# Kernel optimization log

Measured on AMD Instinct MI355X. Metric: run time of the kernel, lower is better.

The kernel has to match this reference:

```python
import jax, jax.numpy as jnp
import numpy as np

OUT, IN, GS = 11008, 4096, 128   # out_features, in_features, group_size
G = IN // GS                     # num_groups = 32 (in_features divisible by group_size)
TOKENS = 8192                    # batch 4 * seq 2048


def setup_inputs() -> dict:
    key = jax.random.key(0)
    k1, k2, k3, k4, k5 = jax.random.split(key, 5)
    x = jax.random.normal(k1, (TOKENS, IN), dtype=jnp.float32)
    # packed int4 weights: two nibbles per byte, stored as int32 in [0,256)
    qweight = jax.random.randint(k2, (OUT, IN // 2), 0, 256, dtype=jnp.int32)
    # realistic GPTQ scales (small positive) and zero-points in [0,15]
    scales = jax.random.uniform(k3, (OUT, G), dtype=jnp.float32) * 0.01 + 1e-3
    zeros = jax.random.uniform(k4, (OUT, G), dtype=jnp.float32) * 15.0
    bias = jax.random.normal(k5, (OUT,), dtype=jnp.float32) * 0.01
    return {"x": x, "qweight": qweight, "scales": scales, "zeros": zeros, "bias": bias}


def _dequant(qweight, scales, zeros):
    # unpack: column 2i = low nibble, column 2i+1 = high nibble (matches torch loop)
    low = (qweight & 15).astype(jnp.float32)          # [OUT, IN/2]
    high = ((qweight >> 4) & 15).astype(jnp.float32)  # [OUT, IN/2]
    w = jnp.stack([low, high], axis=-1).reshape(OUT, IN)
    # group-wise dequant: (q - zero) * scale per group of GS input channels
    w = (w.reshape(OUT, G, GS) - zeros[:, :, None]) * scales[:, :, None]
    return w.reshape(OUT, IN)


def reference(x, qweight, scales, zeros, bias):
    w = _dequant(qweight, scales, zeros)   # [OUT, IN] fp32
    # F.linear: x @ w.T + bias
    return jnp.einsum('ti,oi->to', x, w) + bias
```

## Files before the change

kernel.cpp:

```cpp
#include <hip/hip_runtime.h>
#include <stdint.h>

#define OUTF 11008
#define INF  4096
#define NG   32
#define TOK  8192
#define KB4  2048

#define BM 256
#define BN 256
#define BK 64
#define NT (INF / BK)
#define GX (OUTF / BN)
#define GY (TOK / BM)
#define NWG (GX * GY)

typedef unsigned short u16;
typedef __attribute__((ext_vector_type(8))) short bf16x8;
typedef __attribute__((ext_vector_type(4))) float f32x4;

__device__ inline u16 f2bf(float f) {
  union { float f; uint32_t u; } v; v.f = f;
  return (u16)((v.u + 0x7fff + ((v.u >> 16) & 1)) >> 16);
}

__device__ inline void async_copy16(const void* g, const void* l) {
  __builtin_amdgcn_global_load_lds(
      (__attribute__((address_space(1))) void*)(g),
      (__attribute__((address_space(3))) void*)(l), 16, 0, 0);
}

#define FENCE() asm volatile("" ::: "memory")
#define BAR()   do { FENCE(); __builtin_amdgcn_s_barrier(); FENCE(); } while (0)
#define VMCNT(n) asm volatile("s_waitcnt vmcnt(" #n ")" ::: "memory")


__global__ void dequant_w(const int* __restrict__ QW, const float* __restrict__ scales,
                          const float* __restrict__ zeros, u16* __restrict__ Wb) {
  const int idx = blockIdx.x * 256 + threadIdx.x;
  const int e = idx * 8;
  const int o = e >> 11;
  const int c = e & (KB4 - 1);
  const int g = c >> 6;
  const float s = scales[o * NG + g];
  const float z = zeros[o * NG + g];
  const float zs = -z * s;
#pragma unroll
  for (int h = 0; h < 2; ++h) {
    const int4 q = *(const int4*)(QW + (size_t)o * KB4 + c + h * 4);
    const int qq[4] = {q.x, q.y, q.z, q.w};
    union { u16 t[8]; int4 v; } u;
#pragma unroll
    for (int j = 0; j < 4; ++j) {
      u.t[2 * j]     = f2bf(fmaf((float)(qq[j] & 15), s, zs));
      u.t[2 * j + 1] = f2bf(fmaf((float)((qq[j] >> 4) & 15), s, zs));
    }
    *(int4*)(Wb + (size_t)o * INF + 2 * (c + h * 4)) = u.v;
  }
}

__global__ void cvt_x(const float* __restrict__ X, u16* __restrict__ Xb) {
  const size_t base = ((size_t)blockIdx.x * 256 + threadIdx.x) * 16;
#pragma unroll
  for (int h = 0; h < 2; ++h) {
    const float4 a = *(const float4*)(X + base + h * 8);
    const float4 b = *(const float4*)(X + base + h * 8 + 4);
    union { u16 t[8]; int4 v; } u;
    u.t[0] = f2bf(a.x); u.t[1] = f2bf(a.y); u.t[2] = f2bf(a.z); u.t[3] = f2bf(a.w);
    u.t[4] = f2bf(b.x); u.t[5] = f2bf(b.y); u.t[6] = f2bf(b.z); u.t[7] = f2bf(b.w);
    *(int4*)(Xb + base + h * 8) = u.v;
  }
}


__global__ __launch_bounds__(512, 2) void gemm_pre512(const u16* __restrict__ A,
                                                      const u16* __restrict__ B,
                                                      const float* __restrict__ bias,
                                                      float* __restrict__ C) {
  __shared__ __align__(16) u16 As[2][BM * BK];
  __shared__ __align__(16) u16 Bs[2][BN * BK];
  const int tid = threadIdx.x;
  const int lane = tid & 63;
  const int wid = __builtin_amdgcn_readfirstlane(tid >> 6);

  const int lin = blockIdx.x;
  const int wg = (lin & 7) * (NWG / 8) + (lin >> 3);
  const int bm = wg / GX;
  const int bn = wg % GX;

  const u16* Ab = A + (size_t)bm * BM * INF;
  const u16* Bb = B + (size_t)bn * BN * INF;

  const int rowoff = tid >> 3;
  const int gran = (tid & 7) ^ (rowoff & 7);
  const u16* Asrc = Ab + (size_t)rowoff * INF + gran * 8;
  const u16* Bsrc = Bb + (size_t)rowoff * INF + gran * 8;
  const int wid8 = wid * 8;

  const int rr = lane & 15;
  const int q4 = lane >> 4;
  const int wm = wid >> 2;
  const int wn = wid & 3;

  f32x4 acc[8][4] = {};
  bf16x8 af[8][2], bfv[4][2];

#define STAGE_A(S, TT)                                                         \
  _Pragma("unroll") for (int r0 = 0; r0 < BM; r0 += 64)                        \
    async_copy16(Asrc + (size_t)r0 * INF + (TT) * BK,                          \
                 (const char*)&As[S][0] + (r0 + wid8) * 128);
#define STAGE_B(S, TT)                                                         \
  _Pragma("unroll") for (int r0 = 0; r0 < BN; r0 += 64)                        \
    async_copy16(Bsrc + (size_t)r0 * INF + (TT) * BK,                          \
                 (const char*)&Bs[S][0] + (r0 + wid8) * 128);

#define LD_A(S, MH)                                                            \
  _Pragma("unroll") for (int mi = 0; mi < 4; ++mi)                             \
    _Pragma("unroll") for (int ks = 0; ks < 2; ++ks)                           \
      af[(MH) * 4 + mi][ks] = *(const bf16x8*)&As[S][                          \
          (wm * 128 + ((MH) * 4 + mi) * 16 + rr) * BK +                        \
          (((ks * 4 + q4) ^ (rr & 7)) * 8)];
#define LD_B(S, NH)                                                            \
  _Pragma("unroll") for (int ni = 0; ni < 2; ++ni)                             \
    _Pragma("unroll") for (int ks = 0; ks < 2; ++ks)                           \
      bfv[(NH) * 2 + ni][ks] = *(const bf16x8*)&Bs[S][                         \
          (wn * 64 + ((NH) * 2 + ni) * 16 + rr) * BK +                         \
          (((ks * 4 + q4) ^ (rr & 7)) * 8)];

#define MFMAQ(MH, NH)                                                          \
  do {                                                                         \
    __builtin_amdgcn_s_setprio(1);                                             \
    _Pragma("unroll") for (int ks = 0; ks < 2; ++ks)                           \
      _Pragma("unroll") for (int mi = 0; mi < 4; ++mi)                         \
        _Pragma("unroll") for (int ni = 0; ni < 2; ++ni)                       \
          acc[(MH) * 4 + mi][(NH) * 2 + ni] =                                  \
              __builtin_amdgcn_mfma_f32_16x16x32_bf16(                         \
                  af[(MH) * 4 + mi][ks], bfv[(NH) * 2 + ni][ks],               \
                  acc[(MH) * 4 + mi][(NH) * 2 + ni], 0, 0, 0);                 \
    __builtin_amdgcn_s_setprio(0);                                             \
  } while (0)

#define TILE(S, T)                                                             \
  do {                                                                         \
    LD_A(S, 0); LD_B(S, 0);                                                    \
    BAR(); MFMAQ(0, 0); BAR();                                                 \
    LD_A(S, 1); LD_B(S, 1);                                                    \
    BAR(); MFMAQ(0, 1); BAR();                                                 \
    if ((T) < NT - 2) { STAGE_A(S, (T) + 2); }                                 \
    BAR(); MFMAQ(1, 0); BAR();                                                 \
    if ((T) < NT - 2) { STAGE_B(S, (T) + 2); VMCNT(8); } else { VMCNT(0); }    \
    BAR(); MFMAQ(1, 1); BAR();                                                 \
  } while (0)

  STAGE_A(0, 0); STAGE_B(0, 0);
  STAGE_A(1, 1); STAGE_B(1, 1);
  VMCNT(8);
  BAR();

  for (int t = 0; t < NT; t += 2) {
    TILE(0, t);
    TILE(1, t + 1);
  }

  const int ncol = lane & 15;
  const int qrow = (lane >> 4) * 4;
  float bv[4];
#pragma unroll
  for (int ni = 0; ni < 4; ++ni)
    bv[ni] = bias[bn * BN + wn * 64 + ni * 16 + ncol];
#pragma unroll
  for (int mi = 0; mi < 8; ++mi)
#pragma unroll
    for (int ni = 0; ni < 4; ++ni) {
      const int gn = bn * BN + wn * 64 + ni * 16 + ncol;
#pragma unroll
      for (int r = 0; r < 4; ++r) {
        const int gm = bm * BM + wm * 128 + mi * 16 + qrow + r;
        C[(size_t)gm * OUTF + gn] = acc[mi][ni][r] + bv[ni];
      }
    }
}


#define FBM 128
#define FBN 128

#define FMFMA_COMPUTE()                                                       \
  do {                                                                        \
    const int frr = lane & 15;                                                \
    const int fq4 = lane >> 4;                                                \
    _Pragma("unroll") for (int ks = 0; ks < 2; ++ks) {                        \
      bf16x8 fa[4], fb[4];                                                    \
      const int kk = (((ks * 4 + fq4) ^ (frr & 7)) * 8);                      \
      _Pragma("unroll") for (int i = 0; i < 4; ++i) {                         \
        fa[i] = *(const bf16x8*)&Asf[(mwave + i * 16 + frr) * BK + kk];       \
        fb[i] = *(const bf16x8*)&Bsf[(nwave + i * 16 + frr) * BK + kk];       \
      }                                                                       \
      _Pragma("unroll") for (int mi = 0; mi < 4; ++mi)                        \
        _Pragma("unroll") for (int ni = 0; ni < 4; ++ni)                      \
          facc[mi][ni] = __builtin_amdgcn_mfma_f32_16x16x32_bf16(             \
              fa[mi], fb[ni], facc[mi][ni], 0, 0, 0);                         \
    }                                                                         \
  } while (0)

__global__ __launch_bounds__(256) void gemm_fused(const float* __restrict__ X,
                                                  const int* __restrict__ QW,
                                                  const float* __restrict__ scales,
                                                  const float* __restrict__ zeros,
                                                  const float* __restrict__ bias,
                                                  float* __restrict__ C) {
  __shared__ __align__(16) u16 Asf[FBM * BK];
  __shared__ __align__(16) u16 Bsf[FBN * BK];
  const int tid = threadIdx.x;
  const int lane = tid & 63;
  const int wid = tid >> 6;
  const int bm = blockIdx.y, bn = blockIdx.x;
  const int row = tid >> 1;
  const int half = tid & 1;
  const float* xr = X + (size_t)(bm * FBM + row) * INF + half * 32;
  const int* qr = QW + (size_t)(bn * FBN + row) * KB4 + half * 16;
  const float* srow = scales + (size_t)(bn * FBN + row) * NG;
  const float* zrow = zeros + (size_t)(bn * FBN + row) * NG;
  const int mwave = (wid >> 1) * 64;
  const int nwave = (wid & 1) * 64;
  f32x4 facc[4][4] = {};

  for (int kb = 0; kb < INF / BK; ++kb) {
    const int k0 = kb * BK;
    union { u16 t[32]; int4 v[4]; } ta, tb;
#pragma unroll
    for (int j = 0; j < 8; ++j) {
      const float4 f = *(const float4*)(xr + k0 + j * 4);
      ta.t[4 * j]     = f2bf(f.x);
      ta.t[4 * j + 1] = f2bf(f.y);
      ta.t[4 * j + 2] = f2bf(f.z);
      ta.t[4 * j + 3] = f2bf(f.w);
    }
    {
      const float s = srow[kb >> 1];
      const float zs = -zrow[kb >> 1] * s;
#pragma unroll
      for (int j = 0; j < 4; ++j) {
        const int4 q = *(const int4*)(qr + kb * 32 + j * 4);
        const int qq[4] = {q.x, q.y, q.z, q.w};
#pragma unroll
        for (int u = 0; u < 4; ++u) {
          tb.t[8 * j + 2 * u]     = f2bf(fmaf((float)(qq[u] & 15), s, zs));
          tb.t[8 * j + 2 * u + 1] = f2bf(fmaf((float)((qq[u] >> 4) & 15), s, zs));
        }
      }
    }
    __syncthreads();
#pragma unroll
    for (int j = 0; j < 4; ++j) {
      *(int4*)&Asf[row * BK + (((half * 4 + j) ^ (row & 7)) * 8)] = ta.v[j];
      *(int4*)&Bsf[row * BK + (((half * 4 + j) ^ (row & 7)) * 8)] = tb.v[j];
    }
    __syncthreads();
    FMFMA_COMPUTE();
  }
  {
    const int ncol = lane & 15;
    const int qrow = (lane >> 4) * 4;
#pragma unroll
    for (int mi = 0; mi < 4; ++mi)
#pragma unroll
      for (int ni = 0; ni < 4; ++ni) {
        const int gn = bn * FBN + nwave + ni * 16 + ncol;
        const float bvv = bias[gn];
#pragma unroll
        for (int r = 0; r < 4; ++r) {
          const int gm = bm * FBM + mwave + mi * 16 + qrow + r;
          C[(size_t)gm * OUTF + gn] = facc[mi][ni][r] + bvv;
        }
      }
  }
}


extern "C" void kernel_launch(void* const* d_in, const int* in_sizes, int n_in,
                              void* d_out, int out_size, void* d_ws, size_t ws_size,
                              hipStream_t stream) {
  const float* x = (const float*)d_in[0];
  const int* qw = (const int*)d_in[1];
  const float* scales = (const float*)d_in[2];
  const float* zeros = (const float*)d_in[3];
  const float* bias = (const float*)d_in[4];
  float* out = (float*)d_out;

  const size_t needW = (size_t)OUTF * INF * sizeof(u16);
  const size_t needX = (size_t)TOK * INF * sizeof(u16);

  if (ws_size >= needW + needX) {
    u16* Wb = (u16*)d_ws;
    u16* Xb = (u16*)((char*)d_ws + needW);
    dequant_w<<<(OUTF * KB4 / 8) / 256, 256, 0, stream>>>(qw, scales, zeros, Wb);
    cvt_x<<<(TOK * INF / 16) / 256, 256, 0, stream>>>(x, Xb);
    gemm_pre512<<<dim3(NWG), 512, 0, stream>>>(Xb, Wb, bias, out);
  } else {
    gemm_fused<<<dim3(OUTF / FBN, TOK / FBM), 256, 0, stream>>>(x, qw, scales, zeros, bias, out);
  }
}
```

Baseline: 1.236 ms.

## Restructure GEMM main loop into k-split phases with staggered async staging

The 512-thread bf16 GEMM main loop now reads LDS fragments per k-substep instead of holding both k halves in registers. The fragment register arrays shrink from af[8][2]/bfv[4][2] to af[4]/bfv[4], and each phase waits on lgkmcnt before its MFMAs. Global-to-LDS staging is also rescheduled: half of tile t+1's A rows are issued early, and the other half together with B for t+2 are issued later, with a different vmcnt threshold. The aim is to lower register pressure and spread memory traffic more evenly, at the cost of more barriers and more LDS reads of B.

```diff
diff --git a/kernel.cpp b/kernel.cpp
--- a/kernel.cpp
+++ b/kernel.cpp
@@ -33,6 +33,7 @@
 #define FENCE() asm volatile("" ::: "memory")
 #define BAR()   do { FENCE(); __builtin_amdgcn_s_barrier(); FENCE(); } while (0)
 #define VMCNT(n) asm volatile("s_waitcnt vmcnt(" #n ")" ::: "memory")
+#define LGKM0()  asm volatile("s_waitcnt lgkmcnt(0)" ::: "memory")
 
 
 __global__ void dequant_w(const int* __restrict__ QW, const float* __restrict__ scales,
@@ -103,58 +104,73 @@
   const int wn = wid & 3;
 
   f32x4 acc[8][4] = {};
-  bf16x8 af[8][2], bfv[4][2];
-
-#define STAGE_A(S, TT)                                                         \
-  _Pragma("unroll") for (int r0 = 0; r0 < BM; r0 += 64)                        \
-    async_copy16(Asrc + (size_t)r0 * INF + (TT) * BK,                          \
-                 (const char*)&As[S][0] + (r0 + wid8) * 128);
-#define STAGE_B(S, TT)                                                         \
-  _Pragma("unroll") for (int r0 = 0; r0 < BN; r0 += 64)                        \
-    async_copy16(Bsrc + (size_t)r0 * INF + (TT) * BK,                          \
-                 (const char*)&Bs[S][0] + (r0 + wid8) * 128);
-
-#define LD_A(S, MH)                                                            \
+  bf16x8 af[4];
+  bf16x8 bfv[4];
+
+#define STAGE1(LDS, SRC, TT, R0)                                               \
+  async_copy16((SRC) + (size_t)(R0) * INF + (size_t)(TT) * BK,                 \
+               (const char*)(LDS) + ((R0) + wid8) * 128);
+
+#define PH_READ_A(S, KS, MH)                                                   \
   _Pragma("unroll") for (int mi = 0; mi < 4; ++mi)                             \
-    _Pragma("unroll") for (int ks = 0; ks < 2; ++ks)                           \
-      af[(MH) * 4 + mi][ks] = *(const bf16x8*)&As[S][                          \
-          (wm * 128 + ((MH) * 4 + mi) * 16 + rr) * BK +                        \
-          (((ks * 4 + q4) ^ (rr & 7)) * 8)];
-#define LD_B(S, NH)                                                            \
-  _Pragma("unroll") for (int ni = 0; ni < 2; ++ni)                             \
-    _Pragma("unroll") for (int ks = 0; ks < 2; ++ks)                           \
-      bfv[(NH) * 2 + ni][ks] = *(const bf16x8*)&Bs[S][                         \
-          (wn * 64 + ((NH) * 2 + ni) * 16 + rr) * BK +                         \
-          (((ks * 4 + q4) ^ (rr & 7)) * 8)];
-
-#define MFMAQ(MH, NH)                                                          \
+    af[mi] = *(const bf16x8*)&As[S][(wm * 128 + ((MH) * 4 + mi) * 16 + rr) *   \
+                                        BK +                                   \
+                                    ((((KS) * 4 + q4) ^ (rr & 7)) * 8)];
+
+#define PH_READ_B(S, KS)                                                       \
+  _Pragma("unroll") for (int ni = 0; ni < 4; ++ni)                             \
+    bfv[ni] = *(const bf16x8*)&Bs[S][(wn * 64 + ni * 16 + rr) * BK +           \
+                                     ((((KS) * 4 + q4) ^ (rr & 7)) * 8)];
+
+#define PH_MFMA(MH)                                                            \
   do {                                                                         \
     __builtin_amdgcn_s_setprio(1);                                             \
-    _Pragma("unroll") for (int ks = 0; ks < 2; ++ks)                           \
-      _Pragma("unroll") for (int mi = 0; mi < 4; ++mi)                         \
-        _Pragma("unroll") for (int ni = 0; ni < 2; ++ni)                       \
-          acc[(MH) * 4 + mi][(NH) * 2 + ni] =                                  \
-              __builtin_amdgcn_mfma_f32_16x16x32_bf16(                         \
-                  af[(MH) * 4 + mi][ks], bfv[(NH) * 2 + ni][ks],               \
-                  acc[(MH) * 4 + mi][(NH) * 2 + ni], 0, 0, 0);                 \
+    _Pragma("unroll") for (int mi = 0; mi < 4; ++mi)                           \
+      _Pragma("unroll") for (int ni = 0; ni < 4; ++ni)                         \
+        acc[(MH) * 4 + mi][ni] = __builtin_amdgcn_mfma_f32_16x16x32_bf16(      \
+            af[mi], bfv[ni], acc[(MH) * 4 + mi][ni], 0, 0, 0);                 \
     __builtin_amdgcn_s_setprio(0);                                             \
   } while (0)
 
 #define TILE(S, T)                                                             \
   do {                                                                         \
-    LD_A(S, 0); LD_B(S, 0);                                                    \
-    BAR(); MFMAQ(0, 0); BAR();                                                 \
-    LD_A(S, 1); LD_B(S, 1);                                                    \
-    BAR(); MFMAQ(0, 1); BAR();                                                 \
-    if ((T) < NT - 2) { STAGE_A(S, (T) + 2); }                                 \
-    BAR(); MFMAQ(1, 0); BAR();                                                 \
-    if ((T) < NT - 2) { STAGE_B(S, (T) + 2); VMCNT(8); } else { VMCNT(0); }    \
-    BAR(); MFMAQ(1, 1); BAR();                                                 \
+                                                            \
+    PH_READ_A(S, 0, 0); PH_READ_B(S, 0);                                       \
+    if ((T) + 1 < NT) {                                                        \
+      STAGE1(&As[(S) ^ 1][0], Asrc, (T) + 1, 64)                               \
+      STAGE1(&As[(S) ^ 1][0], Asrc, (T) + 1, 192)                              \
+    }                                                                          \
+    BAR(); LGKM0(); PH_MFMA(0); BAR();                                         \
+                                                            \
+    PH_READ_A(S, 0, 1);                                                        \
+    BAR(); LGKM0(); PH_MFMA(1); BAR();                                         \
+                                                            \
+    PH_READ_A(S, 1, 0); PH_READ_B(S, 1);                                       \
+    BAR(); LGKM0(); PH_MFMA(0); BAR();                                         \
+                                                            \
+    PH_READ_A(S, 1, 1);                                                        \
+    if ((T) + 2 < NT) {                                                        \
+      STAGE1(&As[S][0], Asrc, (T) + 2, 0)                                      \
+      STAGE1(&As[S][0], Asrc, (T) + 2, 128)                                    \
+      STAGE1(&Bs[S][0], Bsrc, (T) + 2, 0)                                      \
+      STAGE1(&Bs[S][0], Bsrc, (T) + 2, 64)                                     \
+      STAGE1(&Bs[S][0], Bsrc, (T) + 2, 128)                                    \
+      STAGE1(&Bs[S][0], Bsrc, (T) + 2, 192)                                    \
+      VMCNT(6);                                                                \
+    } else {                                                                   \
+      VMCNT(0);                                                                \
+    }                                                                          \
+    BAR(); LGKM0(); PH_MFMA(1); BAR();                                         \
   } while (0)
 
-  STAGE_A(0, 0); STAGE_B(0, 0);
-  STAGE_A(1, 1); STAGE_B(1, 1);
-  VMCNT(8);
+  STAGE1(&As[0][0], Asrc, 0, 0)   STAGE1(&As[0][0], Asrc, 0, 64)
+  STAGE1(&As[0][0], Asrc, 0, 128) STAGE1(&As[0][0], Asrc, 0, 192)
+  STAGE1(&Bs[0][0], Bsrc, 0, 0)   STAGE1(&Bs[0][0], Bsrc, 0, 64)
+  STAGE1(&Bs[0][0], Bsrc, 0, 128) STAGE1(&Bs[0][0], Bsrc, 0, 192)
+  STAGE1(&As[1][0], Asrc, 1, 0)   STAGE1(&As[1][0], Asrc, 1, 128)
+  STAGE1(&Bs[1][0], Bsrc, 1, 0)   STAGE1(&Bs[1][0], Bsrc, 1, 64)
+  STAGE1(&Bs[1][0], Bsrc, 1, 128) STAGE1(&Bs[1][0], Bsrc, 1, 192)
+  VMCNT(6);
   BAR();
 
   for (int t = 0; t < NT; t += 2) {
@@ -298,6 +314,6 @@
     cvt_x<<<(TOK * INF / 16) / 256, 256, 0, stream>>>(x, Xb);
     gemm_pre512<<<dim3(NWG), 512, 0, stream>>>(Xb, Wb, bias, out);
   } else {
-    gemm_fused<<<dim3(OUTF / FBN, TOK / FBM), 256, 0, stream>>>(x, qw, scales, zeros, bias, out);
-  }
-}
+    gemm_fused<<<dim3(OUTF / FBN, FBM ? TOK / FBM : 1), 256, 0, stream>>>(x, qw, scales, zeros, bias, out);
+  }
+}
```

Result: slower. 1.304 ms (+5.5%).
